# Kernel optimization log

Hardware: AMD Instinct MI355X
Metric: run time of the kernel (lower is better)

Reference implementation:

```python
import jax, jax.numpy as jnp
import numpy as np

NUM_TOKENS = 8192
NUM_KEYS = 3
TOKEN_DIM = 256
BATCH = 8192
EPS = 1e-12  # F.normalize default eps


def setup_inputs() -> dict:
    key = jax.random.key(0)
    k1, k2, k3, k4, k5 = jax.random.split(key, 5)
    return {
        "new_tokens": jax.random.normal(k1, (BATCH, TOKEN_DIM), jnp.float32),
        "ref_pts": jax.random.uniform(k2, (BATCH, 3), jnp.float32),
        "mem_keys": jax.random.normal(k3, (NUM_TOKENS, NUM_KEYS, TOKEN_DIM), jnp.float32),
        "mem_tokens": jax.random.normal(k4, (NUM_TOKENS, TOKEN_DIM), jnp.float32),
        "mem_ages": jax.random.uniform(k5, (NUM_TOKENS,), jnp.float32) * 10.0,
    }


def reference(new_tokens, ref_pts, mem_keys, mem_tokens, mem_ages):
    B, D = new_tokens.shape
    ages = mem_ages + 1.0  # self.ages += 1

    # torch.cdist(ref_pts, ref_pts, p=2) with inf diagonal
    sq = jnp.sum(ref_pts * ref_pts, axis=1)  # [B]
    d2 = sq[:, None] + sq[None, :] - 2.0 * (ref_pts @ ref_pts.T)
    dists = jnp.sqrt(jnp.maximum(d2, 0.0))
    idx = jnp.arange(B)
    dists = dists.at[idx, idx].set(jnp.inf)
    # argsort(dim=1)[:, :num_keys] == indices of the NUM_KEYS smallest per row
    _, closest_idx = jax.lax.top_k(-dists, NUM_KEYS)  # [B, NUM_KEYS] int32

    # expand new tokens into keys and concatenate with memory
    new_keys = jnp.broadcast_to(new_tokens[:, None, :], (B, NUM_KEYS, D))
    all_keys = jnp.concatenate([mem_keys, new_keys], axis=0)      # [N+B, K, D]
    all_tokens = jnp.concatenate([mem_tokens, new_tokens], axis=0)  # [N+B, D]
    all_ages = jnp.concatenate([ages, jnp.zeros((B,), ages.dtype)], axis=0)

    # cosine-similarity diversity score
    nrm = jnp.maximum(jnp.linalg.norm(all_tokens, axis=1, keepdims=True), EPS)
    norm_tokens = all_tokens / nrm
    cos = norm_tokens @ norm_tokens.T  # [(N+B), (N+B)] -- dominant cost
    diversity = -jnp.sum(cos, axis=1)
    combined = diversity + all_ages

    # topk smallest num_tokens scores, then gather memory entries
    _, keep = jax.lax.top_k(-combined, NUM_TOKENS)
    return all_keys[keep], all_tokens[keep], all_ages[keep], closest_idx
```

## Files before the change

### kernel.cpp

```cpp
#include <hip/hip_runtime.h>
#include <climits>

#define B    8192
#define D    256
#define TOT  16384
#define GS   16
#define NC   (GS * GS * GS)
#define NCH  32
#define JCW  (TOT / NCH)
#define RPB  128


__device__ __forceinline__ int clamp_cell(float x) {
    int c = (int)(x * (float)GS);
    if (c < 0) c = 0;
    if (c > GS - 1) c = GS - 1;
    return c;
}

__global__ void norms_grid(const float* __restrict__ mem_tokens,
                           const float* __restrict__ new_tokens,
                           const float* __restrict__ ref,
                           double* __restrict__ invn, double* __restrict__ S_part,
                           float4* __restrict__ sorted_pts4, int* __restrict__ sorted_idx,
                           int* __restrict__ startg) {
    __shared__ double sacc[4][256];
    __shared__ int cnt_s[NC];
    __shared__ int part[256];
    if (blockIdx.x < 128) {
        int wave = threadIdx.x >> 6;
        int lane = threadIdx.x & 63;
        int rbase = blockIdx.x * RPB;
        double a0 = 0.0, a1 = 0.0, a2 = 0.0, a3 = 0.0;
        for (int k = wave; k < RPB; k += 4) {
            int r = rbase + k;
            const float* row = (r < B) ? (mem_tokens + (size_t)r * D) : (new_tokens + (size_t)(r - B) * D);
            float4 v = *(const float4*)(row + lane * 4);
            double s = (double)v.x * (double)v.x + (double)v.y * (double)v.y +
                       (double)v.z * (double)v.z + (double)v.w * (double)v.w;
            for (int off = 32; off; off >>= 1) s += __shfl_xor(s, off, 64);
            double n = sqrt(s);
            if (n < 1e-12) n = 1e-12;
            double inv = 1.0 / n;
            if (lane == 0) invn[r] = inv;
            a0 += (double)v.x * inv; a1 += (double)v.y * inv;
            a2 += (double)v.z * inv; a3 += (double)v.w * inv;
        }
        sacc[wave][lane * 4 + 0] = a0;
        sacc[wave][lane * 4 + 1] = a1;
        sacc[wave][lane * 4 + 2] = a2;
        sacc[wave][lane * 4 + 3] = a3;
        __syncthreads();
        int d = threadIdx.x;
        S_part[blockIdx.x * 256 + d] = sacc[0][d] + sacc[1][d] + sacc[2][d] + sacc[3][d];
    } else {
        int tid = threadIdx.x;
        for (int c = tid; c < NC; c += 256) cnt_s[c] = 0;
        __syncthreads();
        for (int k = 0; k < 32; ++k) {
            int i = k * 256 + tid;
            int cx = clamp_cell(ref[i * 3 + 0]);
            int cy = clamp_cell(ref[i * 3 + 1]);
            int cz = clamp_cell(ref[i * 3 + 2]);
            atomicAdd(&cnt_s[(cz * GS + cy) * GS + cx], 1);
        }
        __syncthreads();
        int s = 0;
        for (int k = 0; k < 16; ++k) s += cnt_s[tid * 16 + k];
        part[tid] = s;
        __syncthreads();
        if (tid == 0) {
            int acc = 0;
            for (int q = 0; q < 256; ++q) { int v = part[q]; part[q] = acc; acc += v; }
        }
        __syncthreads();
        int base = part[tid];
        for (int k = 0; k < 16; ++k) {
            int c = tid * 16 + k;
            int v = cnt_s[c];
            startg[c] = base;
            cnt_s[c] = base;
            base += v;
        }
        if (tid == 0) startg[NC] = B;
        __syncthreads();
        for (int k = 0; k < 32; ++k) {
            int i = k * 256 + tid;
            float x = ref[i * 3 + 0], y = ref[i * 3 + 1], z = ref[i * 3 + 2];
            int c = (clamp_cell(z) * GS + clamp_cell(y)) * GS + clamp_cell(x);
            float sq = __fadd_rn(__fadd_rn(__fmul_rn(x, x), __fmul_rn(y, y)), __fmul_rn(z, z));
            int pos = atomicAdd(&cnt_s[c], 1);
            sorted_pts4[pos] = make_float4(x, y, z, sq);
            sorted_idx[pos]  = i;
        }
    }
}

__global__ void knn_sreduce(const float4* __restrict__ sorted_pts4,
                            const int* __restrict__ sorted_idx,
                            const int* __restrict__ start,
                            float* __restrict__ out_closest,
                            const double* __restrict__ S_part, double* __restrict__ S) {
    if (blockIdx.x == 2048) {
        int d = threadIdx.x;
        double s = 0.0;
        for (int b = 0; b < TOT / RPB; ++b) s += S_part[b * 256 + d];
        S[d] = s;
        return;
    }
    int wave = threadIdx.x >> 6;
    int lane = threadIdx.x & 63;
    int k = blockIdx.x * 4 + wave;
    float4 q = sorted_pts4[k];
    int i = sorted_idx[k];
    int cx = clamp_cell(q.x), cy = clamp_cell(q.y), cz = clamp_cell(q.z);
    const float h = 1.0f / (float)GS, eps = 1e-3f;
    float w0 = INFINITY, w1 = INFINITY, w2 = INFINITY;
    int   wi0 = INT_MAX, wi1 = INT_MAX, wi2 = INT_MAX;
    int R = 0;
    while (true) {
        ++R;
        float b0 = INFINITY, b1 = INFINITY, b2 = INFINITY;
        int   i0 = INT_MAX, i1 = INT_MAX, i2 = INT_MAX;
        int xlo = max(cx - R, 0), xhi = min(cx + R, GS - 1);
        int ylo = max(cy - R, 0), yhi = min(cy + R, GS - 1);
        int zlo = max(cz - R, 0), zhi = min(cz + R, GS - 1);
        int ny = yhi - ylo + 1;
        int rows = ny * (zhi - zlo + 1);
        for (int r = lane; r < rows; r += 64) {
            int z = zlo + r / ny;
            int y = ylo + r % ny;
            int crow = (z * GS + y) * GS;
            int s = start[crow + xlo];
            int e = start[crow + xhi + 1];
            for (int t = s; t < e; ++t) {
                int j = sorted_idx[t];
                if (j == i) continue;
                float4 p = sorted_pts4[t];
                float dot = __fmaf_rn(q.z, p.z, __fmaf_rn(q.y, p.y, __fmul_rn(q.x, p.x)));
                float d2  = __fsub_rn(__fadd_rn(q.w, p.w), __fmul_rn(2.0f, dot));
                float d   = __fsqrt_rn(fmaxf(d2, 0.0f));
                bool lt2 = (d < b2) || (d == b2 && j < i2);
                if (lt2) {
                    bool lt1 = (d < b1) || (d == b1 && j < i1);
                    if (lt1) {
                        b2 = b1; i2 = i1;
                        bool lt0 = (d < b0) || (d == b0 && j < i0);
                        if (lt0) { b1 = b0; i1 = i0; b0 = d; i0 = j; }
                        else     { b1 = d; i1 = j; }
                    } else { b2 = d; i2 = j; }
                }
            }
        }
        #pragma unroll
        for (int s = 0; s < 3; ++s) {
            float d = b0; int ix = i0;
            for (int off = 32; off; off >>= 1) {
                float od = __shfl_xor(d, off, 64);
                int   oi = __shfl_xor(ix, off, 64);
                if (od < d || (od == d && oi < ix)) { d = od; ix = oi; }
            }
            if (s == 0) { w0 = d; wi0 = ix; }
            else if (s == 1) { w1 = d; wi1 = ix; }
            else { w2 = d; wi2 = ix; }
            if (i0 == ix) { b0 = b1; i0 = i1; b1 = b2; i1 = i2; b2 = INFINITY; i2 = INT_MAX; }
        }
        bool covers = (xlo == 0 && ylo == 0 && zlo == 0 &&
                       xhi == GS - 1 && yhi == GS - 1 && zhi == GS - 1);
        if (covers) break;
        if (wi2 != INT_MAX && w2 < (float)R * h - eps) break;
    }
    if (lane == 0) {
        out_closest[i * 3 + 0] = (float)wi0;
        out_closest[i * 3 + 1] = (float)wi1;
        out_closest[i * 3 + 2] = (float)wi2;
    }
}

__global__ void combined_kernel(const float* __restrict__ mem_tokens, const float* __restrict__ new_tokens,
                                const float* __restrict__ mem_ages,
                                const double* __restrict__ invn, const double* __restrict__ S,
                                double* __restrict__ comb) {
    int wave = threadIdx.x >> 6;
    int lane = threadIdx.x & 63;
    int r = blockIdx.x * 4 + wave;
    const float* row = (r < B) ? (mem_tokens + (size_t)r * D) : (new_tokens + (size_t)(r - B) * D);
    float4 v = *(const float4*)(row + lane * 4);
    const double* Sp = S + lane * 4;
    double s = (double)v.x * Sp[0] + (double)v.y * Sp[1] +
               (double)v.z * Sp[2] + (double)v.w * Sp[3];
    for (int off = 32; off; off >>= 1) s += __shfl_down(s, off, 64);
    if (lane == 0) {
        double age = (r < B) ? (double)mem_ages[r] + 1.0 : 0.0;
        comb[r] = age - s * invn[r];
    }
}

__global__ void rank_count(const double* __restrict__ comb, int* __restrict__ partial) {
    __shared__ double cl[JCW];
    int tid  = threadIdx.x;
    int base = (blockIdx.x * 256 + tid) * 4;
    int j0   = blockIdx.y * JCW;
    for (int t = tid; t < JCW; t += 256) cl[t] = comb[j0 + t];
    __syncthreads();
    double c0 = comb[base + 0], c1 = comb[base + 1];
    double c2 = comb[base + 2], c3 = comb[base + 3];
    int n0 = 0, n1 = 0, n2 = 0, n3 = 0;
    int lo = base - j0;       if (lo < 0) lo = 0; if (lo > JCW) lo = JCW;
    int hi = base + 4 - j0;   if (hi < 0) hi = 0; if (hi > JCW) hi = JCW;
    #pragma unroll 8
    for (int t = 0; t < lo; ++t) {
        double cj = cl[t];
        n0 += (cj <= c0); n1 += (cj <= c1); n2 += (cj <= c2); n3 += (cj <= c3);
    }
    for (int t = lo; t < hi; ++t) {
        double cj = cl[t];
        int j = j0 + t;
        n0 += (cj < c0) || (cj == c0 && j < base + 0);
        n1 += (cj < c1) || (cj == c1 && j < base + 1);
        n2 += (cj < c2) || (cj == c2 && j < base + 2);
        n3 += (cj < c3) || (cj == c3 && j < base + 3);
    }
    #pragma unroll 8
    for (int t = hi; t < JCW; ++t) {
        double cj = cl[t];
        n0 += (cj < c0); n1 += (cj < c1); n2 += (cj < c2); n3 += (cj < c3);
    }
    *(int4*)&partial[blockIdx.y * TOT + base] = make_int4(n0, n1, n2, n3);
}

__global__ void gather(const float* __restrict__ mem_keys, const float* __restrict__ mem_tokens,
                       const float* __restrict__ new_tokens, const float* __restrict__ mem_ages,
                       const int* __restrict__ partial,
                       float* __restrict__ out_keys, float* __restrict__ out_tokens,
                       float* __restrict__ out_ages) {
    __shared__ int psum[32];
    int r = blockIdx.x;
    int t = threadIdx.x;
    if (t < 32) psum[t] = partial[t * TOT + r];
    __syncthreads();
    if (t < 8) {
        int s = psum[t] + psum[t + 8] + psum[t + 16] + psum[t + 24];
        psum[t] = s;
    }
    __syncthreads();
    if (t == 0) {
        psum[0] = psum[0] + psum[1] + psum[2] + psum[3] +
                  psum[4] + psum[5] + psum[6] + psum[7];
    }
    __syncthreads();
    int rk = psum[0];
    if (rk >= B) return;
    float4* ot = (float4*)(out_tokens + (size_t)rk * D);
    float4* ok = (float4*)(out_keys + (size_t)rk * 3 * D);
    if (r < B) {
        if (t < 64) {
            const float4* st = (const float4*)(mem_tokens + (size_t)r * D);
            ot[t] = st[t];
        } else {
            const float4* sk = (const float4*)(mem_keys + (size_t)r * 3 * D);
            ok[t - 64] = sk[t - 64];
        }
        if (t == 0) out_ages[rk] = mem_ages[r] + 1.0f;
    } else {
        const float4* nt = (const float4*)(new_tokens + (size_t)(r - B) * D);
        float4 v = nt[t & 63];
        if (t < 64) ot[t] = v;
        else        ok[t - 64] = v;
        if (t == 0) out_ages[rk] = 0.0f;
    }
}

extern "C" void kernel_launch(void* const* d_in, const int* in_sizes, int n_in,
                              void* d_out, int out_size, void* d_ws, size_t ws_size,
                              hipStream_t stream) {
    const float* new_tokens = (const float*)d_in[0];
    const float* ref_pts    = (const float*)d_in[1];
    const float* mem_keys   = (const float*)d_in[2];
    const float* mem_tokens = (const float*)d_in[3];
    const float* mem_ages   = (const float*)d_in[4];

    char* ws = (char*)d_ws;
    float4* sorted_pts4 = (float4*)(ws + 0);
    int*    sorted_idx  = (int*)   (ws + 131072);
    int*    startg      = (int*)   (ws + 163840);
    double* invn        = (double*)(ws + 196608);
    double* S_part      = (double*)(ws + 327680);
    double* S           = (double*)(ws + 589824);
    double* comb        = (double*)(ws + 591872);
    int*    partial     = (int*)   (ws + 722944);

    float* out = (float*)d_out;
    float* out_keys    = out;
    float* out_tokens  = out + 6291456;
    float* out_ages    = out + 6291456 + 2097152;
    float* out_closest = out_ages + 8192;

    norms_grid<<<129, 256, 0, stream>>>(mem_tokens, new_tokens, ref_pts,
                                        invn, S_part, sorted_pts4, sorted_idx, startg);
    knn_sreduce<<<2049, 256, 0, stream>>>(sorted_pts4, sorted_idx, startg,
                                          out_closest, S_part, S);
    combined_kernel<<<TOT / 4, 256, 0, stream>>>(mem_tokens, new_tokens, mem_ages, invn, S, comb);
    rank_count<<<dim3(TOT / (256 * 4), NCH), 256, 0, stream>>>(comb, partial);
    gather<<<TOT, 256, 0, stream>>>(mem_keys, mem_tokens, new_tokens, mem_ages, partial,
                                    out_keys, out_tokens, out_ages);
}
```

Before: 92.81 us.

## Fuse combined-score computation into knn kernel and halve rows per norms block

The standalone combined_kernel launch is removed. Its work moves into 128 extra blocks of the knn kernel, and each of those blocks first reduces S_part into shared memory, so the separate S reduction and one launch are gone and the score work runs alongside the KNN search. The norms kernel now processes 64 rows per block across 256 blocks, which gives more parallelism in exchange for twice as many S_part partials that each extra block must sum. The redundant per-block summation of 256 partials adds global reads.

```diff
diff --git a/kernel.cpp b/kernel.cpp
--- a/kernel.cpp
+++ b/kernel.cpp
@@ -8,7 +8,8 @@
 #define NC   (GS * GS * GS)
 #define NCH  32
 #define JCW  (TOT / NCH)
-#define RPB  128
+#define RPB  64
+#define NSB  (TOT / RPB)
 
 
 __device__ __forceinline__ int clamp_cell(float x) {
@@ -27,7 +28,7 @@
     __shared__ double sacc[4][256];
     __shared__ int cnt_s[NC];
     __shared__ int part[256];
-    if (blockIdx.x < 128) {
+    if (blockIdx.x < NSB) {
         int wave = threadIdx.x >> 6;
         int lane = threadIdx.x & 63;
         int rbase = blockIdx.x * RPB;
@@ -96,20 +97,41 @@
     }
 }
 
-__global__ void knn_sreduce(const float4* __restrict__ sorted_pts4,
-                            const int* __restrict__ sorted_idx,
-                            const int* __restrict__ start,
-                            float* __restrict__ out_closest,
-                            const double* __restrict__ S_part, double* __restrict__ S) {
-    if (blockIdx.x == 2048) {
-        int d = threadIdx.x;
-        double s = 0.0;
-        for (int b = 0; b < TOT / RPB; ++b) s += S_part[b * 256 + d];
-        S[d] = s;
-        return;
-    }
+__global__ void knn_combined(const float4* __restrict__ sorted_pts4,
+                             const int* __restrict__ sorted_idx,
+                             const int* __restrict__ start,
+                             float* __restrict__ out_closest,
+                             const float* __restrict__ mem_tokens,
+                             const float* __restrict__ new_tokens,
+                             const float* __restrict__ mem_ages,
+                             const double* __restrict__ invn,
+                             const double* __restrict__ S_part,
+                             double* __restrict__ comb) {
+    __shared__ double Sl[256];
     int wave = threadIdx.x >> 6;
     int lane = threadIdx.x & 63;
+    if (blockIdx.x >= 2048) {
+        int tid = threadIdx.x;
+        double s = 0.0;
+        for (int b = 0; b < NSB; ++b) s += S_part[b * 256 + tid];
+        Sl[tid] = s;
+        __syncthreads();
+        int rbase = (blockIdx.x - 2048) * 128;
+        for (int k = wave; k < 128; k += 4) {
+            int r = rbase + k;
+            const float* row = (r < B) ? (mem_tokens + (size_t)r * D) : (new_tokens + (size_t)(r - B) * D);
+            float4 v = *(const float4*)(row + lane * 4);
+            const double* Sp = Sl + lane * 4;
+            double acc = (double)v.x * Sp[0] + (double)v.y * Sp[1] +
+                         (double)v.z * Sp[2] + (double)v.w * Sp[3];
+            for (int off = 32; off; off >>= 1) acc += __shfl_down(acc, off, 64);
+            if (lane == 0) {
+                double age = (r < B) ? (double)mem_ages[r] + 1.0 : 0.0;
+                comb[r] = age - acc * invn[r];
+            }
+        }
+        return;
+    }
     int k = blockIdx.x * 4 + wave;
     float4 q = sorted_pts4[k];
     int i = sorted_idx[k];
@@ -177,25 +199,6 @@
     }
 }
 
-__global__ void combined_kernel(const float* __restrict__ mem_tokens, const float* __restrict__ new_tokens,
-                                const float* __restrict__ mem_ages,
-                                const double* __restrict__ invn, const double* __restrict__ S,
-                                double* __restrict__ comb) {
-    int wave = threadIdx.x >> 6;
-    int lane = threadIdx.x & 63;
-    int r = blockIdx.x * 4 + wave;
-    const float* row = (r < B) ? (mem_tokens + (size_t)r * D) : (new_tokens + (size_t)(r - B) * D);
-    float4 v = *(const float4*)(row + lane * 4);
-    const double* Sp = S + lane * 4;
-    double s = (double)v.x * Sp[0] + (double)v.y * Sp[1] +
-               (double)v.z * Sp[2] + (double)v.w * Sp[3];
-    for (int off = 32; off; off >>= 1) s += __shfl_down(s, off, 64);
-    if (lane == 0) {
-        double age = (r < B) ? (double)mem_ages[r] + 1.0 : 0.0;
-        comb[r] = age - s * invn[r];
-    }
-}
-
 __global__ void rank_count(const double* __restrict__ comb, int* __restrict__ partial) {
     __shared__ double cl[JCW];
     int tid  = threadIdx.x;
@@ -286,9 +289,8 @@
     int*    startg      = (int*)   (ws + 163840);
     double* invn        = (double*)(ws + 196608);
     double* S_part      = (double*)(ws + 327680);
-    double* S           = (double*)(ws + 589824);
-    double* comb        = (double*)(ws + 591872);
-    int*    partial     = (int*)   (ws + 722944);
+    double* comb        = (double*)(ws + 851968);
+    int*    partial     = (int*)   (ws + 983040);
 
     float* out = (float*)d_out;
     float* out_keys    = out;
@@ -296,11 +298,11 @@
     float* out_ages    = out + 6291456 + 2097152;
     float* out_closest = out_ages + 8192;
 
-    norms_grid<<<129, 256, 0, stream>>>(mem_tokens, new_tokens, ref_pts,
-                                        invn, S_part, sorted_pts4, sorted_idx, startg);
-    knn_sreduce<<<2049, 256, 0, stream>>>(sorted_pts4, sorted_idx, startg,
-                                          out_closest, S_part, S);
-    combined_kernel<<<TOT / 4, 256, 0, stream>>>(mem_tokens, new_tokens, mem_ages, invn, S, comb);
+    norms_grid<<<NSB + 1, 256, 0, stream>>>(mem_tokens, new_tokens, ref_pts,
+                                            invn, S_part, sorted_pts4, sorted_idx, startg);
+    knn_combined<<<2048 + 128, 256, 0, stream>>>(sorted_pts4, sorted_idx, startg, out_closest,
+                                                 mem_tokens, new_tokens, mem_ages, invn,
+                                                 S_part, comb);
     rank_count<<<dim3(TOT / (256 * 4), NCH), 256, 0, stream>>>(comb, partial);
     gather<<<TOT, 256, 0, stream>>>(mem_keys, mem_tokens, new_tokens, mem_ages, partial,
                                     out_keys, out_tokens, out_ages);
```

After: 125.2 us. 1.35x slower.
